# Kernel tuning notes

Hardware: AMD Instinct MI355X
Metric: run time of the kernel (lower is better)

Reference implementation:

```python
import math
import jax, jax.numpy as jnp
import numpy as np

EMB = 1024
HEADS = 16
HD = EMB // HEADS  # 64
MAXPOS = 1024
BATCH = 4
SEQ = 1024


def get_rope_cache(dim, max_pos, theta=10000.0):
    # NOTE: faithfully reproduces the (i - 1) quirk of the source (not the standard i)
    i = jnp.arange(dim // 2, dtype=jnp.float32)
    theta_i = theta ** (-2.0 * (i - 1.0) / dim)
    pos = jnp.arange(max_pos, dtype=jnp.float32)[:, None]
    th = pos * theta_i  # [max_pos, dim//2]
    return jnp.stack([jnp.cos(th), jnp.sin(th)], axis=-1)  # [max_pos, dim//2, 2]


def apply_rope(x, rope_cache):
    # x: [B, H, S, hd]. Source casts pairs to float16 before the complex multiply,
    # then the complex32*complex64 product promotes back to float32 -> emulate via
    # an fp16 round-trip on x, with the rotation itself done in fp32.
    B, H, S, hd = x.shape
    rc = rope_cache[:S]  # [S, hd//2, 2]
    xp = x.reshape(B, H, S, hd // 2, 2).astype(jnp.float16).astype(jnp.float32)
    a, b = xp[..., 0], xp[..., 1]
    cos, sin = rc[..., 0], rc[..., 1]
    rot = jnp.stack([a * cos - b * sin, a * sin + b * cos], axis=-1)
    return rot.reshape(B, H, S, hd)


def setup_inputs() -> dict:
    key = jax.random.key(0)
    ks = jax.random.split(key, 5)
    std = math.sqrt(2.0 / (EMB + EMB))
    x = jax.random.normal(ks[0], (BATCH, SEQ, EMB), dtype=jnp.float32)
    padding_mask = jnp.ones((BATCH, SEQ), dtype=jnp.float32)
    Wq = jax.random.normal(ks[1], (EMB, EMB), dtype=jnp.float32) * std
    Wk = jax.random.normal(ks[2], (EMB, EMB), dtype=jnp.float32) * std
    Wv = jax.random.normal(ks[3], (EMB, EMB), dtype=jnp.float32) * std
    Wo = jax.random.normal(ks[4], (EMB, EMB), dtype=jnp.float32) * std
    rope_cache = get_rope_cache(HD, MAXPOS)
    return {"x": x, "padding_mask": padding_mask, "Wq": Wq, "Wk": Wk,
            "Wv": Wv, "Wo": Wo, "rope_cache": rope_cache}


def reference(x, padding_mask, Wq, Wk, Wv, Wo, rope_cache):
    B, S, E = x.shape

    def heads(t):  # [B,S,E] -> [B,H,S,hd]
        return t.reshape(B, S, HEADS, HD).transpose(0, 2, 1, 3)

    q = heads(x @ Wq.T)
    k = heads(x @ Wk.T)
    v = heads(x @ Wv.T)
    q = apply_rope(q, rope_cache)
    k = apply_rope(k, rope_cache)

    scores = jnp.einsum('bhqd,bhkd->bhqk', q, k)  # [B,H,S,S]
    causal = jnp.tril(jnp.ones((S, S), jnp.float32))
    mask = (causal[None, :, :] * padding_mask[:, None, :])[:, None]  # [B,1,S,S]
    scores = jnp.where(mask == 0, jnp.float32(-1e9), scores) / math.sqrt(HD)
    weights = jax.nn.softmax(scores, axis=-1)

    out = jnp.einsum('bhqk,bhkd->bhqd', weights, v)  # [B,H,S,hd]
    # Faithful to source: transpose(-2,-1) then .view(B,S,-1) scrambles head_dim/seq
    out = out.transpose(0, 1, 3, 2).reshape(B, S, E)
    return out @ Wo.T
```

## Files before the change

### kernel.cpp

```cpp
#include <hip/hip_runtime.h>

#define SEQ   1024
#define HEADS 16
#define HD    64
#define BATCH 4
#define EMB   1024

typedef __attribute__((ext_vector_type(8))) short  short8;
typedef __attribute__((ext_vector_type(4))) float  floatx4;

__device__ __forceinline__ unsigned short f2bf(float f) {
    unsigned u = __builtin_bit_cast(unsigned, f);
    u += 0x7FFF + ((u >> 16) & 1);
    return (unsigned short)(u >> 16);
}

__device__ __forceinline__ void g2l16(const void* g, void* l) {
    __builtin_amdgcn_global_load_lds((const __attribute__((address_space(1))) unsigned int*)g,
                                     (__attribute__((address_space(3))) unsigned int*)l,
                                     16, 0, 0);
}

__device__ __forceinline__ short8 ldsfrag(const unsigned short* base, int row, int cq) {
    int ch = cq ^ (row & 7);
    return *(const short8*)(base + row * 64 + ch * 8);
}

__global__ __launch_bounds__(256) void cvt_kernel(
    const float* __restrict__ x,  const float* __restrict__ wq,
    const float* __restrict__ wk, const float* __restrict__ wv,
    const float* __restrict__ wo,
    unsigned short* __restrict__ xb,  unsigned short* __restrict__ wqb,
    unsigned short* __restrict__ wkb, unsigned short* __restrict__ wvb,
    unsigned short* __restrict__ wob) {
    int blk = blockIdx.x;
    const float* src; unsigned short* dst; int rel;
    if      (blk < 4096) { src = x;  dst = xb;  rel = blk; }
    else if (blk < 5120) { src = wq; dst = wqb; rel = blk - 4096; }
    else if (blk < 6144) { src = wk; dst = wkb; rel = blk - 5120; }
    else if (blk < 7168) { src = wv; dst = wvb; rel = blk - 6144; }
    else                 { src = wo; dst = wob; rel = blk - 7168; }
    size_t i = (size_t)rel * 1024 + threadIdx.x * 4;
    float4 v = *(const float4*)(src + i);
    ushort4 o;
    o.x = f2bf(v.x); o.y = f2bf(v.y); o.z = f2bf(v.z); o.w = f2bf(v.w);
    *(ushort4*)(dst + i) = o;
}

template<int MODE>
__global__ __launch_bounds__(256) void gemm_m97(
    const unsigned short* __restrict__ A, const unsigned short* __restrict__ W,
    void* __restrict__ out0, void* __restrict__ out1, void* __restrict__ out2,
    const float* __restrict__ rc, int M, int N, int K) {
    __shared__ unsigned short As[128 * 64];
    __shared__ unsigned short Bs[128 * 64];
    const int tid  = threadIdx.x;
    const int lane = tid & 63;
    const int wid  = tid >> 6;
    const int l15  = lane & 15, quad = lane >> 4;
    const int wm   = (wid & 1) * 64, wn = (wid >> 1) * 64;
    const int m0   = blockIdx.y * 128, n0 = blockIdx.x * 128;
    const int boff = tid * 16;

    floatx4 acc[4][4] = {};
    const char* Ab = (const char*)A;
    const char* Wb = (const char*)W;
    const size_t rstride = (size_t)K * 2;

    for (int k0 = 0; k0 < K; k0 += 64) {
#pragma unroll
        for (int c = 0; c < 4; c++) {
            int o = c * 4096 + boff;
            int row = o >> 7;
            int sw  = ((o >> 4) & 7) ^ (row & 7);
            g2l16(Ab + (size_t)(m0 + row) * rstride + (size_t)k0 * 2 + sw * 16, (char*)As + o);
            g2l16(Wb + (size_t)(n0 + row) * rstride + (size_t)k0 * 2 + sw * 16, (char*)Bs + o);
        }
        __syncthreads();
#pragma unroll
        for (int ks = 0; ks < 2; ks++) {
            short8 a[4], b[4];
#pragma unroll
            for (int i = 0; i < 4; i++) a[i] = ldsfrag(As, wm + i * 16 + l15, ks * 4 + quad);
#pragma unroll
            for (int j = 0; j < 4; j++) b[j] = ldsfrag(Bs, wn + j * 16 + l15, ks * 4 + quad);
#pragma unroll
            for (int i = 0; i < 4; i++)
#pragma unroll
                for (int j = 0; j < 4; j++)
                    acc[i][j] = __builtin_amdgcn_mfma_f32_16x16x32_bf16(a[i], b[j], acc[i][j], 0, 0, 0);
        }
        __syncthreads();
    }

    const int which = n0 >> 10;
#pragma unroll
    for (int i = 0; i < 4; i++) {
#pragma unroll
        for (int r = 0; r < 4; r++) {
            int m = m0 + wm + i * 16 + quad * 4 + r;
            int bb = m >> 10, s = m & 1023;
#pragma unroll
            for (int j = 0; j < 4; j++) {
                int n = n0 + wn + j * 16 + l15;
                float v = acc[i][j][r];
                if (MODE == 0) {
                    ((float*)out0)[(size_t)m * N + n] = v;
                } else {
                    int nr = n & 1023, h = nr >> 6, d = nr & 63;
                    if (which < 2) {
                        float vp = __shfl_xor(v, 1);
                        float2 cs = *(const float2*)&rc[(size_t)s * 64 + (d & ~1)];
                        v = (l15 & 1) ? (vp * cs.y + v * cs.x) : (v * cs.x - vp * cs.y);
                        unsigned short* dst = (which == 0) ? (unsigned short*)out0
                                                           : (unsigned short*)out1;
                        dst[(((size_t)bb * HEADS + h) * SEQ + s) * HD + d] = f2bf(v);
                    } else {
                        ((unsigned short*)out2)[(((size_t)bb * HEADS + h) * HD + d) * SEQ + s] = f2bf(v);
                    }
                }
            }
        }
    }
}

__global__ __launch_bounds__(256) void attn_kernel(
    const unsigned short* __restrict__ Qb, const unsigned short* __restrict__ Kb,
    const unsigned short* __restrict__ VTb, const float* __restrict__ pm,
    unsigned short* __restrict__ Tb) {
    __shared__ unsigned short Ks[64 * 64];
    __shared__ unsigned short Vs[64 * 64];
    __shared__ unsigned short Ps[4][16][72];
    __shared__ float pmf[64];
    const int tid  = threadIdx.x;
    const int lane = tid & 63, wid = tid >> 6;
    const int l15  = lane & 15, quad = lane >> 4;
    const int bh   = blockIdx.x, b = bh >> 4;
    const int q0   = (15 - blockIdx.y) * 64;
    const int qw   = q0 + wid * 16;
    const int q    = qw + l15;
    const unsigned short* Qh  = Qb  + (size_t)bh * SEQ * HD;
    const unsigned short* Kh  = Kb  + (size_t)bh * SEQ * HD;
    const unsigned short* VTh = VTb + (size_t)bh * HD * SEQ;
    unsigned short*       Th  = Tb  + (size_t)bh * HD * SEQ;
    const float* pmb = pm + b * SEQ;
    const float SCL2 = 0.125f * 1.44269504088896340736f;

    short8 qf0 = *(const short8*)&Qh[(size_t)q * HD + quad * 8];
    short8 qf1 = *(const short8*)&Qh[(size_t)q * HD + 32 + quad * 8];

    floatx4 ot[4] = {};
    float l_lane = 0.f;
    unsigned short (*Pw)[72] = Ps[wid];
    const int boff = tid * 16;

    for (int kvc = 0; kvc <= q0; kvc += 64) {
        const char* kg = (const char*)(Kh + (size_t)kvc * HD);
        const char* vg = (const char*)(VTh + kvc);
#pragma unroll
        for (int c = 0; c < 2; c++) {
            int o = c * 4096 + boff;
            int row = o >> 7;
            int sw  = ((o >> 4) & 7) ^ (row & 7);
            g2l16(kg + (size_t)row * 128 + sw * 16, (char*)Ks + o);
            g2l16(vg + (size_t)row * (SEQ * 2) + sw * 16, (char*)Vs + o);
        }
        if (tid < 64) pmf[tid] = (pmb[kvc + tid] != 0.f) ? 1.f : 0.f;
        __syncthreads();

        const bool diag = (kvc + 63 > qw);
        floatx4 sc[4];
#pragma unroll
        for (int st = 0; st < 4; st++) {
            short8 ka0 = ldsfrag(Ks, st * 16 + l15, quad);
            short8 ka1 = ldsfrag(Ks, st * 16 + l15, 4 + quad);
            floatx4 z = {0.f, 0.f, 0.f, 0.f};
            z = __builtin_amdgcn_mfma_f32_16x16x32_bf16(ka0, qf0, z, 0, 0, 0);
            z = __builtin_amdgcn_mfma_f32_16x16x32_bf16(ka1, qf1, z, 0, 0, 0);
            sc[st] = z;
        }
#pragma unroll
        for (int st = 0; st < 4; st++) {
            float4 pmv = *(const float4*)&pmf[st * 16 + quad * 4];
            int kvbase = kvc + st * 16 + quad * 4;
            ushort4 pk;
#pragma unroll
            for (int r = 0; r < 4; r++) {
                float e = exp2f(sc[st][r] * SCL2) * ((&pmv.x)[r]);
                if (diag && (kvbase + r > q)) e = 0.f;
                l_lane += e;
                (&pk.x)[r] = f2bf(e);
            }
            *(ushort4*)&Pw[l15][st * 16 + quad * 4] = pk;
        }
        asm volatile("s_waitcnt lgkmcnt(0)" ::: "memory");
        short8 pf0 = *(const short8*)&Pw[l15][quad * 8];
        short8 pf1 = *(const short8*)&Pw[l15][32 + quad * 8];

#pragma unroll
        for (int jt = 0; jt < 4; jt++) {
            short8 v0 = ldsfrag(Vs, jt * 16 + l15, quad);
            short8 v1 = ldsfrag(Vs, jt * 16 + l15, 4 + quad);
            ot[jt] = __builtin_amdgcn_mfma_f32_16x16x32_bf16(v0, pf0, ot[jt], 0, 0, 0);
            ot[jt] = __builtin_amdgcn_mfma_f32_16x16x32_bf16(v1, pf1, ot[jt], 0, 0, 0);
        }
        __syncthreads();
    }

    float l = l_lane;
    l += __shfl_xor(l, 16);
    l += __shfl_xor(l, 32);
    float inv = 1.0f / l;
#pragma unroll
    for (int jt = 0; jt < 4; jt++)
#pragma unroll
        for (int r = 0; r < 4; r++)
            Th[(size_t)(jt * 16 + quad * 4 + r) * SEQ + q] = f2bf(ot[jt][r] * inv);
}

extern "C" void kernel_launch(void* const* d_in, const int* in_sizes, int n_in,
                              void* d_out, int out_size, void* d_ws, size_t ws_size,
                              hipStream_t stream) {
    const float* x  = (const float*)d_in[0];
    const float* pm = (const float*)d_in[1];
    const float* Wq = (const float*)d_in[2];
    const float* Wk = (const float*)d_in[3];
    const float* Wv = (const float*)d_in[4];
    const float* Wo = (const float*)d_in[5];
    const float* rc = (const float*)d_in[6];

    char* base = (char*)d_ws;
    unsigned short* xb   = (unsigned short*)(base);
    unsigned short* wqkv = (unsigned short*)(base + (8u  << 20));
    unsigned short* wob  = (unsigned short*)(base + (14u << 20));
    unsigned short* Qb   = (unsigned short*)(base + (16u << 20));
    unsigned short* Kb   = (unsigned short*)(base + (24u << 20));
    unsigned short* VTb  = (unsigned short*)(base + (32u << 20));
    unsigned short* Tb   = (unsigned short*)(base + (40u << 20));

    cvt_kernel<<<8192, 256, 0, stream>>>(x, Wq, Wk, Wv, Wo,
                                         xb, wqkv, wqkv + (1u << 20), wqkv + (2u << 20), wob);
    gemm_m97<1><<<dim3(24, 32), 256, 0, stream>>>(xb, wqkv, (void*)Qb, (void*)Kb, (void*)VTb,
                                                  rc, 4096, 3072, 1024);
    attn_kernel<<<dim3(64, 16), 256, 0, stream>>>(Qb, Kb, VTb, pm, Tb);
    gemm_m97<0><<<dim3(8, 32), 256, 0, stream>>>(Tb, wob, d_out, nullptr, nullptr,
                                                 nullptr, 4096, 1024, 1024);
}
```

Before: 184.6 us.

## Give each attention wave two query tiles and shrink output GEMM tile

The attention kernel now runs 2 waves per block instead of 4. Each wave handles 32 query rows as two 16-row tiles, so every K and V fragment read from LDS feeds twice as many MFMAs. The GEMM is templated on tile size, and the output projection now uses 128x64 tiles, giving 512 blocks instead of 256 to fill more CUs. The cost is more registers per attention wave and fewer waves per block to hide latency. The smaller output-GEMM tile also lowers arithmetic intensity per block.

```diff
diff --git a/kernel.cpp b/kernel.cpp
--- a/kernel.cpp
+++ b/kernel.cpp
@@ -47,47 +47,54 @@
     *(ushort4*)(dst + i) = o;
 }
 
-template<int MODE>
+template<int MODE, int TM, int TN>
 __global__ __launch_bounds__(256) void gemm_m97(
     const unsigned short* __restrict__ A, const unsigned short* __restrict__ W,
     void* __restrict__ out0, void* __restrict__ out1, void* __restrict__ out2,
     const float* __restrict__ rc, int M, int N, int K) {
-    __shared__ unsigned short As[128 * 64];
-    __shared__ unsigned short Bs[128 * 64];
+    constexpr int IM = TM / 32, JN = TN / 32;
+    __shared__ unsigned short As[TM * 64];
+    __shared__ unsigned short Bs[TN * 64];
     const int tid  = threadIdx.x;
     const int lane = tid & 63;
     const int wid  = tid >> 6;
     const int l15  = lane & 15, quad = lane >> 4;
-    const int wm   = (wid & 1) * 64, wn = (wid >> 1) * 64;
-    const int m0   = blockIdx.y * 128, n0 = blockIdx.x * 128;
+    const int wm   = (wid & 1) * (TM / 2), wn = (wid >> 1) * (TN / 2);
+    const int m0   = blockIdx.y * TM, n0 = blockIdx.x * TN;
     const int boff = tid * 16;
 
-    floatx4 acc[4][4] = {};
+    floatx4 acc[IM][JN] = {};
     const char* Ab = (const char*)A;
     const char* Wb = (const char*)W;
     const size_t rstride = (size_t)K * 2;
 
     for (int k0 = 0; k0 < K; k0 += 64) {
 #pragma unroll
-        for (int c = 0; c < 4; c++) {
+        for (int c = 0; c < TM / 32; c++) {
             int o = c * 4096 + boff;
             int row = o >> 7;
             int sw  = ((o >> 4) & 7) ^ (row & 7);
             g2l16(Ab + (size_t)(m0 + row) * rstride + (size_t)k0 * 2 + sw * 16, (char*)As + o);
+        }
+#pragma unroll
+        for (int c = 0; c < TN / 32; c++) {
+            int o = c * 4096 + boff;
+            int row = o >> 7;
+            int sw  = ((o >> 4) & 7) ^ (row & 7);
             g2l16(Wb + (size_t)(n0 + row) * rstride + (size_t)k0 * 2 + sw * 16, (char*)Bs + o);
         }
         __syncthreads();
 #pragma unroll
         for (int ks = 0; ks < 2; ks++) {
-            short8 a[4], b[4];
-#pragma unroll
-            for (int i = 0; i < 4; i++) a[i] = ldsfrag(As, wm + i * 16 + l15, ks * 4 + quad);
-#pragma unroll
-            for (int j = 0; j < 4; j++) b[j] = ldsfrag(Bs, wn + j * 16 + l15, ks * 4 + quad);
-#pragma unroll
-            for (int i = 0; i < 4; i++)
-#pragma unroll
-                for (int j = 0; j < 4; j++)
+            short8 a[IM], b[JN];
+#pragma unroll
+            for (int i = 0; i < IM; i++) a[i] = ldsfrag(As, wm + i * 16 + l15, ks * 4 + quad);
+#pragma unroll
+            for (int j = 0; j < JN; j++) b[j] = ldsfrag(Bs, wn + j * 16 + l15, ks * 4 + quad);
+#pragma unroll
+            for (int i = 0; i < IM; i++)
+#pragma unroll
+                for (int j = 0; j < JN; j++)
                     acc[i][j] = __builtin_amdgcn_mfma_f32_16x16x32_bf16(a[i], b[j], acc[i][j], 0, 0, 0);
         }
         __syncthreads();
@@ -95,13 +102,13 @@
 
     const int which = n0 >> 10;
 #pragma unroll
-    for (int i = 0; i < 4; i++) {
+    for (int i = 0; i < IM; i++) {
 #pragma unroll
         for (int r = 0; r < 4; r++) {
             int m = m0 + wm + i * 16 + quad * 4 + r;
             int bb = m >> 10, s = m & 1023;
 #pragma unroll
-            for (int j = 0; j < 4; j++) {
+            for (int j = 0; j < JN; j++) {
                 int n = n0 + wn + j * 16 + l15;
                 float v = acc[i][j][r];
                 if (MODE == 0) {
@@ -124,21 +131,20 @@
     }
 }
 
-__global__ __launch_bounds__(256) void attn_kernel(
+__global__ __launch_bounds__(128) void attn_kernel(
     const unsigned short* __restrict__ Qb, const unsigned short* __restrict__ Kb,
     const unsigned short* __restrict__ VTb, const float* __restrict__ pm,
     unsigned short* __restrict__ Tb) {
     __shared__ unsigned short Ks[64 * 64];
     __shared__ unsigned short Vs[64 * 64];
-    __shared__ unsigned short Ps[4][16][72];
+    __shared__ unsigned short Ps[2][2][16][72];
     __shared__ float pmf[64];
     const int tid  = threadIdx.x;
     const int lane = tid & 63, wid = tid >> 6;
     const int l15  = lane & 15, quad = lane >> 4;
     const int bh   = blockIdx.x, b = bh >> 4;
     const int q0   = (15 - blockIdx.y) * 64;
-    const int qw   = q0 + wid * 16;
-    const int q    = qw + l15;
+    const int qw   = q0 + wid * 32;
     const unsigned short* Qh  = Qb  + (size_t)bh * SEQ * HD;
     const unsigned short* Kh  = Kb  + (size_t)bh * SEQ * HD;
     const unsigned short* VTh = VTb + (size_t)bh * HD * SEQ;
@@ -146,20 +152,23 @@
     const float* pmb = pm + b * SEQ;
     const float SCL2 = 0.125f * 1.44269504088896340736f;
 
-    short8 qf0 = *(const short8*)&Qh[(size_t)q * HD + quad * 8];
-    short8 qf1 = *(const short8*)&Qh[(size_t)q * HD + 32 + quad * 8];
-
-    floatx4 ot[4] = {};
-    float l_lane = 0.f;
-    unsigned short (*Pw)[72] = Ps[wid];
+    short8 qf[2][2];
+#pragma unroll
+    for (int u = 0; u < 2; u++) {
+        qf[u][0] = *(const short8*)&Qh[(size_t)(qw + u * 16 + l15) * HD + quad * 8];
+        qf[u][1] = *(const short8*)&Qh[(size_t)(qw + u * 16 + l15) * HD + 32 + quad * 8];
+    }
+
+    floatx4 ot[2][4] = {};
+    float l_lane[2] = {0.f, 0.f};
     const int boff = tid * 16;
 
     for (int kvc = 0; kvc <= q0; kvc += 64) {
         const char* kg = (const char*)(Kh + (size_t)kvc * HD);
         const char* vg = (const char*)(VTh + kvc);
 #pragma unroll
-        for (int c = 0; c < 2; c++) {
-            int o = c * 4096 + boff;
+        for (int c = 0; c < 4; c++) {
+            int o = c * 2048 + boff;
             int row = o >> 7;
             int sw  = ((o >> 4) & 7) ^ (row & 7);
             g2l16(kg + (size_t)row * 128 + sw * 16, (char*)Ks + o);
@@ -168,54 +177,73 @@
         if (tid < 64) pmf[tid] = (pmb[kvc + tid] != 0.f) ? 1.f : 0.f;
         __syncthreads();
 
-        const bool diag = (kvc + 63 > qw);
-        floatx4 sc[4];
+        floatx4 sc[2][4];
 #pragma unroll
         for (int st = 0; st < 4; st++) {
             short8 ka0 = ldsfrag(Ks, st * 16 + l15, quad);
             short8 ka1 = ldsfrag(Ks, st * 16 + l15, 4 + quad);
-            floatx4 z = {0.f, 0.f, 0.f, 0.f};
-            z = __builtin_amdgcn_mfma_f32_16x16x32_bf16(ka0, qf0, z, 0, 0, 0);
-            z = __builtin_amdgcn_mfma_f32_16x16x32_bf16(ka1, qf1, z, 0, 0, 0);
-            sc[st] = z;
-        }
-#pragma unroll
-        for (int st = 0; st < 4; st++) {
-            float4 pmv = *(const float4*)&pmf[st * 16 + quad * 4];
-            int kvbase = kvc + st * 16 + quad * 4;
-            ushort4 pk;
-#pragma unroll
-            for (int r = 0; r < 4; r++) {
-                float e = exp2f(sc[st][r] * SCL2) * ((&pmv.x)[r]);
-                if (diag && (kvbase + r > q)) e = 0.f;
-                l_lane += e;
-                (&pk.x)[r] = f2bf(e);
-            }
-            *(ushort4*)&Pw[l15][st * 16 + quad * 4] = pk;
+#pragma unroll
+            for (int u = 0; u < 2; u++) {
+                floatx4 z = {0.f, 0.f, 0.f, 0.f};
+                z = __builtin_amdgcn_mfma_f32_16x16x32_bf16(ka0, qf[u][0], z, 0, 0, 0);
+                z = __builtin_amdgcn_mfma_f32_16x16x32_bf16(ka1, qf[u][1], z, 0, 0, 0);
+                sc[u][st] = z;
+            }
+        }
+#pragma unroll
+        for (int u = 0; u < 2; u++) {
+            const int qbase = qw + u * 16;
+            const int qq = qbase + l15;
+            const bool diag = (kvc + 63 > qbase);
+#pragma unroll
+            for (int st = 0; st < 4; st++) {
+                float4 pmv = *(const float4*)&pmf[st * 16 + quad * 4];
+                int kvbase = kvc + st * 16 + quad * 4;
+                ushort4 pk;
+#pragma unroll
+                for (int r = 0; r < 4; r++) {
+                    float e = exp2f(sc[u][st][r] * SCL2) * ((&pmv.x)[r]);
+                    if (diag && (kvbase + r > qq)) e = 0.f;
+                    l_lane[u] += e;
+                    (&pk.x)[r] = f2bf(e);
+                }
+                *(ushort4*)&Ps[wid][u][l15][st * 16 + quad * 4] = pk;
+            }
         }
         asm volatile("s_waitcnt lgkmcnt(0)" ::: "memory");
-        short8 pf0 = *(const short8*)&Pw[l15][quad * 8];
-        short8 pf1 = *(const short8*)&Pw[l15][32 + quad * 8];
+        short8 pf[2][2];
+#pragma unroll
+        for (int u = 0; u < 2; u++) {
+            pf[u][0] = *(const short8*)&Ps[wid][u][l15][quad * 8];
+            pf[u][1] = *(const short8*)&Ps[wid][u][l15][32 + quad * 8];
+        }
 
 #pragma unroll
         for (int jt = 0; jt < 4; jt++) {
             short8 v0 = ldsfrag(Vs, jt * 16 + l15, quad);
             short8 v1 = ldsfrag(Vs, jt * 16 + l15, 4 + quad);
-            ot[jt] = __builtin_amdgcn_mfma_f32_16x16x32_bf16(v0, pf0, ot[jt], 0, 0, 0);
-            ot[jt] = __builtin_amdgcn_mfma_f32_16x16x32_bf16(v1, pf1, ot[jt], 0, 0, 0);
-        }
-        __syncthreads();
-    }
-
-    float l = l_lane;
-    l += __shfl_xor(l, 16);
-    l += __shfl_xor(l, 32);
-    float inv = 1.0f / l;
-#pragma unroll
-    for (int jt = 0; jt < 4; jt++)
-#pragma unroll
-        for (int r = 0; r < 4; r++)
-            Th[(size_t)(jt * 16 + quad * 4 + r) * SEQ + q] = f2bf(ot[jt][r] * inv);
+#pragma unroll
+            for (int u = 0; u < 2; u++) {
+                ot[u][jt] = __builtin_amdgcn_mfma_f32_16x16x32_bf16(v0, pf[u][0], ot[u][jt], 0, 0, 0);
+                ot[u][jt] = __builtin_amdgcn_mfma_f32_16x16x32_bf16(v1, pf[u][1], ot[u][jt], 0, 0, 0);
+            }
+        }
+        __syncthreads();
+    }
+
+#pragma unroll
+    for (int u = 0; u < 2; u++) {
+        float l = l_lane[u];
+        l += __shfl_xor(l, 16);
+        l += __shfl_xor(l, 32);
+        float inv = 1.0f / l;
+        int q = qw + u * 16 + l15;
+#pragma unroll
+        for (int jt = 0; jt < 4; jt++)
+#pragma unroll
+            for (int r = 0; r < 4; r++)
+                Th[(size_t)(jt * 16 + quad * 4 + r) * SEQ + q] = f2bf(ot[u][jt][r] * inv);
+    }
 }
 
 extern "C" void kernel_launch(void* const* d_in, const int* in_sizes, int n_in,
@@ -240,9 +268,9 @@
 
     cvt_kernel<<<8192, 256, 0, stream>>>(x, Wq, Wk, Wv, Wo,
                                          xb, wqkv, wqkv + (1u << 20), wqkv + (2u << 20), wob);
-    gemm_m97<1><<<dim3(24, 32), 256, 0, stream>>>(xb, wqkv, (void*)Qb, (void*)Kb, (void*)VTb,
-                                                  rc, 4096, 3072, 1024);
-    attn_kernel<<<dim3(64, 16), 256, 0, stream>>>(Qb, Kb, VTb, pm, Tb);
-    gemm_m97<0><<<dim3(8, 32), 256, 0, stream>>>(Tb, wob, d_out, nullptr, nullptr,
-                                                 nullptr, 4096, 1024, 1024);
-}
+    gemm_m97<1, 128, 128><<<dim3(24, 32), 256, 0, stream>>>(
+        xb, wqkv, (void*)Qb, (void*)Kb, (void*)VTb, rc, 4096, 3072, 1024);
+    attn_kernel<<<dim3(64, 16), 128, 0, stream>>>(Qb, Kb, VTb, pm, Tb);
+    gemm_m97<0, 128, 64><<<dim3(16, 32), 256, 0, stream>>>(
+        Tb, wob, d_out, nullptr, nullptr, nullptr, 4096, 1024, 1024);
+}
```

After: 193.1 us. 1.05x slower.

## Split-K the output projection and load V fragments directly from global

Applied to the files above, without the earlier changes.

The output projection GEMM runs only 256 blocks, so it is split along K into two halves over a grid z dimension. The second half writes to a workspace buffer and a separate kernel adds the two partials. This raises parallelism to fill more CUs, at the cost of an extra launch and additional fp32 traffic. In attention, V fragments are now read straight from global memory into registers instead of staging through LDS, which frees shared memory but loses swizzled, coalesced staging.

```diff
diff --git a/kernel.cpp b/kernel.cpp
--- a/kernel.cpp
+++ b/kernel.cpp
@@ -47,7 +47,7 @@
     *(ushort4*)(dst + i) = o;
 }
 
-template<int MODE>
+template<int MODE, int SPLIT>
 __global__ __launch_bounds__(256) void gemm_m97(
     const unsigned short* __restrict__ A, const unsigned short* __restrict__ W,
     void* __restrict__ out0, void* __restrict__ out1, void* __restrict__ out2,
@@ -61,13 +61,16 @@
     const int wm   = (wid & 1) * 64, wn = (wid >> 1) * 64;
     const int m0   = blockIdx.y * 128, n0 = blockIdx.x * 128;
     const int boff = tid * 16;
+    const int kz   = SPLIT ? blockIdx.z : 0;
+    const int kbeg = SPLIT ? kz * (K / 2) : 0;
+    const int kend = SPLIT ? kbeg + K / 2 : K;
 
     floatx4 acc[4][4] = {};
     const char* Ab = (const char*)A;
     const char* Wb = (const char*)W;
     const size_t rstride = (size_t)K * 2;
 
-    for (int k0 = 0; k0 < K; k0 += 64) {
+    for (int k0 = kbeg; k0 < kend; k0 += 64) {
 #pragma unroll
         for (int c = 0; c < 4; c++) {
             int o = c * 4096 + boff;
@@ -94,6 +97,7 @@
     }
 
     const int which = n0 >> 10;
+    float* fout = (MODE == 0) ? (kz ? (float*)out1 : (float*)out0) : nullptr;
 #pragma unroll
     for (int i = 0; i < 4; i++) {
 #pragma unroll
@@ -105,7 +109,7 @@
                 int n = n0 + wn + j * 16 + l15;
                 float v = acc[i][j][r];
                 if (MODE == 0) {
-                    ((float*)out0)[(size_t)m * N + n] = v;
+                    fout[(size_t)m * N + n] = v;
                 } else {
                     int nr = n & 1023, h = nr >> 6, d = nr & 63;
                     if (which < 2) {
@@ -124,12 +128,20 @@
     }
 }
 
+__global__ __launch_bounds__(256) void addp_kernel(
+    float* __restrict__ out, const float* __restrict__ p1) {
+    size_t i = ((size_t)blockIdx.x * 256 + threadIdx.x) * 4;
+    float4 a = *(const float4*)(out + i);
+    float4 b = *(const float4*)(p1 + i);
+    a.x += b.x; a.y += b.y; a.z += b.z; a.w += b.w;
+    *(float4*)(out + i) = a;
+}
+
 __global__ __launch_bounds__(256) void attn_kernel(
     const unsigned short* __restrict__ Qb, const unsigned short* __restrict__ Kb,
     const unsigned short* __restrict__ VTb, const float* __restrict__ pm,
     unsigned short* __restrict__ Tb) {
     __shared__ unsigned short Ks[64 * 64];
-    __shared__ unsigned short Vs[64 * 64];
     __shared__ unsigned short Ps[4][16][72];
     __shared__ float pmf[64];
     const int tid  = threadIdx.x;
@@ -145,6 +157,7 @@
     unsigned short*       Th  = Tb  + (size_t)bh * HD * SEQ;
     const float* pmb = pm + b * SEQ;
     const float SCL2 = 0.125f * 1.44269504088896340736f;
+    const int boff = tid * 16;
 
     short8 qf0 = *(const short8*)&Qh[(size_t)q * HD + quad * 8];
     short8 qf1 = *(const short8*)&Qh[(size_t)q * HD + 32 + quad * 8];
@@ -152,23 +165,26 @@
     floatx4 ot[4] = {};
     float l_lane = 0.f;
     unsigned short (*Pw)[72] = Ps[wid];
-    const int boff = tid * 16;
 
     for (int kvc = 0; kvc <= q0; kvc += 64) {
         const char* kg = (const char*)(Kh + (size_t)kvc * HD);
-        const char* vg = (const char*)(VTh + kvc);
 #pragma unroll
         for (int c = 0; c < 2; c++) {
             int o = c * 4096 + boff;
             int row = o >> 7;
             int sw  = ((o >> 4) & 7) ^ (row & 7);
             g2l16(kg + (size_t)row * 128 + sw * 16, (char*)Ks + o);
-            g2l16(vg + (size_t)row * (SEQ * 2) + sw * 16, (char*)Vs + o);
         }
         if (tid < 64) pmf[tid] = (pmb[kvc + tid] != 0.f) ? 1.f : 0.f;
         __syncthreads();
 
-        const bool diag = (kvc + 63 > qw);
+        short8 vf[4][2];
+#pragma unroll
+        for (int jt = 0; jt < 4; jt++) {
+            vf[jt][0] = *(const short8*)&VTh[(size_t)(jt * 16 + l15) * SEQ + kvc + quad * 8];
+            vf[jt][1] = *(const short8*)&VTh[(size_t)(jt * 16 + l15) * SEQ + kvc + 32 + quad * 8];
+        }
+
         floatx4 sc[4];
 #pragma unroll
         for (int st = 0; st < 4; st++) {
@@ -179,6 +195,7 @@
             z = __builtin_amdgcn_mfma_f32_16x16x32_bf16(ka1, qf1, z, 0, 0, 0);
             sc[st] = z;
         }
+        const bool diag = (kvc + 63 > qw);
 #pragma unroll
         for (int st = 0; st < 4; st++) {
             float4 pmv = *(const float4*)&pmf[st * 16 + quad * 4];
@@ -199,10 +216,8 @@
 
 #pragma unroll
         for (int jt = 0; jt < 4; jt++) {
-            short8 v0 = ldsfrag(Vs, jt * 16 + l15, quad);
-            short8 v1 = ldsfrag(Vs, jt * 16 + l15, 4 + quad);
-            ot[jt] = __builtin_amdgcn_mfma_f32_16x16x32_bf16(v0, pf0, ot[jt], 0, 0, 0);
-            ot[jt] = __builtin_amdgcn_mfma_f32_16x16x32_bf16(v1, pf1, ot[jt], 0, 0, 0);
+            ot[jt] = __builtin_amdgcn_mfma_f32_16x16x32_bf16(vf[jt][0], pf0, ot[jt], 0, 0, 0);
+            ot[jt] = __builtin_amdgcn_mfma_f32_16x16x32_bf16(vf[jt][1], pf1, ot[jt], 0, 0, 0);
         }
         __syncthreads();
     }
@@ -237,12 +252,19 @@
     unsigned short* Kb   = (unsigned short*)(base + (24u << 20));
     unsigned short* VTb  = (unsigned short*)(base + (32u << 20));
     unsigned short* Tb   = (unsigned short*)(base + (40u << 20));
+    float*          P1   = (float*)(base + (48u << 20));
 
     cvt_kernel<<<8192, 256, 0, stream>>>(x, Wq, Wk, Wv, Wo,
                                          xb, wqkv, wqkv + (1u << 20), wqkv + (2u << 20), wob);
-    gemm_m97<1><<<dim3(24, 32), 256, 0, stream>>>(xb, wqkv, (void*)Qb, (void*)Kb, (void*)VTb,
-                                                  rc, 4096, 3072, 1024);
+    gemm_m97<1, 0><<<dim3(24, 32), 256, 0, stream>>>(
+        xb, wqkv, (void*)Qb, (void*)Kb, (void*)VTb, rc, 4096, 3072, 1024);
     attn_kernel<<<dim3(64, 16), 256, 0, stream>>>(Qb, Kb, VTb, pm, Tb);
-    gemm_m97<0><<<dim3(8, 32), 256, 0, stream>>>(Tb, wob, d_out, nullptr, nullptr,
-                                                 nullptr, 4096, 1024, 1024);
-}
+    if (ws_size >= (64u << 20)) {
+        gemm_m97<0, 1><<<dim3(8, 32, 2), 256, 0, stream>>>(
+            Tb, wob, d_out, (void*)P1, nullptr, nullptr, 4096, 1024, 1024);
+        addp_kernel<<<4096, 256, 0, stream>>>((float*)d_out, P1);
+    } else {
+        gemm_m97<0, 0><<<dim3(8, 32), 256, 0, stream>>>(
+            Tb, wob, d_out, nullptr, nullptr, nullptr, 4096, 1024, 1024);
+    }
+}
```

After: 206.1 us. 1.12x slower.

## Split attention KV chunks across waves with LDS reduction and 16-query blocks

Applied to the files above, without the earlier changes.

Attention blocks now handle 16 queries each, and the four waves split the causal KV chunks between them (split-K). Each wave loads K and V fragments directly from global memory instead of staging them in shared memory, then the partial outputs and row sums are reduced through LDS. This aims to raise parallelism and remove block-wide barriers. In exchange, K/V reads are repeated across more blocks and waves sit idle on short causal rows.

```diff
diff --git a/kernel.cpp b/kernel.cpp
--- a/kernel.cpp
+++ b/kernel.cpp
@@ -128,17 +128,17 @@
     const unsigned short* __restrict__ Qb, const unsigned short* __restrict__ Kb,
     const unsigned short* __restrict__ VTb, const float* __restrict__ pm,
     unsigned short* __restrict__ Tb) {
-    __shared__ unsigned short Ks[64 * 64];
-    __shared__ unsigned short Vs[64 * 64];
+    __shared__ float Of[4][64][17];
+    __shared__ float lw[4][16];
     __shared__ unsigned short Ps[4][16][72];
-    __shared__ float pmf[64];
+    __shared__ float pmf[SEQ];
     const int tid  = threadIdx.x;
     const int lane = tid & 63, wid = tid >> 6;
     const int l15  = lane & 15, quad = lane >> 4;
     const int bh   = blockIdx.x, b = bh >> 4;
-    const int q0   = (15 - blockIdx.y) * 64;
-    const int qw   = q0 + wid * 16;
-    const int q    = qw + l15;
+    const int tq   = 63 - blockIdx.y;
+    const int q0   = tq * 16;
+    const int q    = q0 + l15;
     const unsigned short* Qh  = Qb  + (size_t)bh * SEQ * HD;
     const unsigned short* Kh  = Kb  + (size_t)bh * SEQ * HD;
     const unsigned short* VTh = VTb + (size_t)bh * HD * SEQ;
@@ -146,42 +146,54 @@
     const float* pmb = pm + b * SEQ;
     const float SCL2 = 0.125f * 1.44269504088896340736f;
 
+    {
+        float4 pv = *(const float4*)&pmb[tid * 4];
+        float4 o;
+        o.x = (pv.x != 0.f) ? 1.f : 0.f; o.y = (pv.y != 0.f) ? 1.f : 0.f;
+        o.z = (pv.z != 0.f) ? 1.f : 0.f; o.w = (pv.w != 0.f) ? 1.f : 0.f;
+        *(float4*)&pmf[tid * 4] = o;
+    }
+    __syncthreads();
+
     short8 qf0 = *(const short8*)&Qh[(size_t)q * HD + quad * 8];
     short8 qf1 = *(const short8*)&Qh[(size_t)q * HD + 32 + quad * 8];
 
     floatx4 ot[4] = {};
     float l_lane = 0.f;
     unsigned short (*Pw)[72] = Ps[wid];
-    const int boff = tid * 16;
-
-    for (int kvc = 0; kvc <= q0; kvc += 64) {
-        const char* kg = (const char*)(Kh + (size_t)kvc * HD);
-        const char* vg = (const char*)(VTh + kvc);
-#pragma unroll
-        for (int c = 0; c < 2; c++) {
-            int o = c * 4096 + boff;
-            int row = o >> 7;
-            int sw  = ((o >> 4) & 7) ^ (row & 7);
-            g2l16(kg + (size_t)row * 128 + sw * 16, (char*)Ks + o);
-            g2l16(vg + (size_t)row * (SEQ * 2) + sw * 16, (char*)Vs + o);
-        }
-        if (tid < 64) pmf[tid] = (pmb[kvc + tid] != 0.f) ? 1.f : 0.f;
-        __syncthreads();
-
-        const bool diag = (kvc + 63 > qw);
+
+    const int nch  = (tq >> 2) + 1;
+    const int icd  = tq >> 2;
+
+    for (int ic = wid; ic < nch; ic += 4) {
+        const int kvc = ic * 64;
+        short8 ka[4][2], vv[4][2];
+#pragma unroll
+        for (int st = 0; st < 4; st++) {
+            const unsigned short* kr = Kh + (size_t)(kvc + st * 16 + l15) * HD;
+            ka[st][0] = *(const short8*)(kr + quad * 8);
+            ka[st][1] = *(const short8*)(kr + 32 + quad * 8);
+        }
+#pragma unroll
+        for (int jt = 0; jt < 4; jt++) {
+            const unsigned short* vr = VTh + (size_t)(jt * 16 + l15) * SEQ + kvc;
+            vv[jt][0] = *(const short8*)(vr + quad * 8);
+            vv[jt][1] = *(const short8*)(vr + 32 + quad * 8);
+        }
+
         floatx4 sc[4];
 #pragma unroll
         for (int st = 0; st < 4; st++) {
-            short8 ka0 = ldsfrag(Ks, st * 16 + l15, quad);
-            short8 ka1 = ldsfrag(Ks, st * 16 + l15, 4 + quad);
             floatx4 z = {0.f, 0.f, 0.f, 0.f};
-            z = __builtin_amdgcn_mfma_f32_16x16x32_bf16(ka0, qf0, z, 0, 0, 0);
-            z = __builtin_amdgcn_mfma_f32_16x16x32_bf16(ka1, qf1, z, 0, 0, 0);
+            z = __builtin_amdgcn_mfma_f32_16x16x32_bf16(ka[st][0], qf0, z, 0, 0, 0);
+            z = __builtin_amdgcn_mfma_f32_16x16x32_bf16(ka[st][1], qf1, z, 0, 0, 0);
             sc[st] = z;
         }
+
+        const bool diag = (ic == icd);
 #pragma unroll
         for (int st = 0; st < 4; st++) {
-            float4 pmv = *(const float4*)&pmf[st * 16 + quad * 4];
+            float4 pmv = *(const float4*)&pmf[kvc + st * 16 + quad * 4];
             int kvbase = kvc + st * 16 + quad * 4;
             ushort4 pk;
 #pragma unroll
@@ -199,23 +211,32 @@
 
 #pragma unroll
         for (int jt = 0; jt < 4; jt++) {
-            short8 v0 = ldsfrag(Vs, jt * 16 + l15, quad);
-            short8 v1 = ldsfrag(Vs, jt * 16 + l15, 4 + quad);
-            ot[jt] = __builtin_amdgcn_mfma_f32_16x16x32_bf16(v0, pf0, ot[jt], 0, 0, 0);
-            ot[jt] = __builtin_amdgcn_mfma_f32_16x16x32_bf16(v1, pf1, ot[jt], 0, 0, 0);
-        }
-        __syncthreads();
+            ot[jt] = __builtin_amdgcn_mfma_f32_16x16x32_bf16(vv[jt][0], pf0, ot[jt], 0, 0, 0);
+            ot[jt] = __builtin_amdgcn_mfma_f32_16x16x32_bf16(vv[jt][1], pf1, ot[jt], 0, 0, 0);
+        }
     }
 
     float l = l_lane;
     l += __shfl_xor(l, 16);
     l += __shfl_xor(l, 32);
-    float inv = 1.0f / l;
+    if (lane < 16) lw[wid][lane] = l;
 #pragma unroll
     for (int jt = 0; jt < 4; jt++)
 #pragma unroll
         for (int r = 0; r < 4; r++)
-            Th[(size_t)(jt * 16 + quad * 4 + r) * SEQ + q] = f2bf(ot[jt][r] * inv);
+            Of[wid][jt * 16 + quad * 4 + r][l15] = ot[jt][r];
+    __syncthreads();
+
+    {
+        float L = lw[0][l15] + lw[1][l15] + lw[2][l15] + lw[3][l15];
+        float invL = 1.0f / L;
+#pragma unroll
+        for (int r = 0; r < 4; r++) {
+            int d = wid * 16 + quad * 4 + r;
+            float s = Of[0][d][l15] + Of[1][d][l15] + Of[2][d][l15] + Of[3][d][l15];
+            Th[(size_t)d * SEQ + q0 + l15] = f2bf(s * invL);
+        }
+    }
 }
 
 extern "C" void kernel_launch(void* const* d_in, const int* in_sizes, int n_in,
@@ -240,9 +261,9 @@
 
     cvt_kernel<<<8192, 256, 0, stream>>>(x, Wq, Wk, Wv, Wo,
                                          xb, wqkv, wqkv + (1u << 20), wqkv + (2u << 20), wob);
-    gemm_m97<1><<<dim3(24, 32), 256, 0, stream>>>(xb, wqkv, (void*)Qb, (void*)Kb, (void*)VTb,
-                                                  rc, 4096, 3072, 1024);
-    attn_kernel<<<dim3(64, 16), 256, 0, stream>>>(Qb, Kb, VTb, pm, Tb);
-    gemm_m97<0><<<dim3(8, 32), 256, 0, stream>>>(Tb, wob, d_out, nullptr, nullptr,
-                                                 nullptr, 4096, 1024, 1024);
-}
+    gemm_m97<1><<<dim3(24, 32), 256, 0, stream>>>(
+        xb, wqkv, (void*)Qb, (void*)Kb, (void*)VTb, rc, 4096, 3072, 1024);
+    attn_kernel<<<dim3(64, 64), 256, 0, stream>>>(Qb, Kb, VTb, pm, Tb);
+    gemm_m97<0><<<dim3(8, 32), 256, 0, stream>>>(
+        Tb, wob, d_out, nullptr, nullptr, nullptr, 4096, 1024, 1024);
+}
```

Result: slower. 223.0 us (+20.8%).
